# Kernel optimization log

Measured on AMD Instinct MI355X. Metric: run time of the kernel, lower is better.

## Reference

```python
import jax, jax.numpy as jnp
import numpy as np

N = 65536      # occupied voxels
D = 96         # voxel grid extent per axis
CIN = 64
CH = 64
COUT = 16      # 8 * 2
K = 27         # 3^3 kernel offsets


def _build_neighbor_idx(rng):
    # unique occupied voxel coordinates
    lin = rng.choice(D ** 3, size=N, replace=False).astype(np.int64)
    coords = np.stack(np.unravel_index(lin, (D, D, D)), axis=1)  # [N,3]
    grid = np.full(D ** 3, -1, dtype=np.int32)
    grid[lin] = np.arange(N, dtype=np.int32)
    # 27 offsets in {-1,0,1}^3 (MinkowskiEngine kernel map, stride 1)
    offs = np.stack(np.meshgrid(*([np.arange(-1, 2)] * 3), indexing='ij'),
                    axis=-1).reshape(K, 3)
    nc = coords[:, None, :] + offs[None, :, :]            # [N,27,3]
    valid = np.all((nc >= 0) & (nc < D), axis=-1)         # [N,27]
    nlin = (nc[..., 0] * D + nc[..., 1]) * D + nc[..., 2]
    nidx = np.where(valid, grid[np.clip(nlin, 0, D ** 3 - 1)], -1)
    return nidx.astype(np.int32)                          # -1 = no neighbor


def setup_inputs() -> dict:
    key = jax.random.key(0)
    ks = jax.random.split(key, 7)
    rng = np.random.default_rng(0)
    neighbor_idx = jnp.asarray(_build_neighbor_idx(rng))
    s1 = 1.0 / np.sqrt(K * CIN)
    s2 = 1.0 / np.sqrt(K * CH)
    return {
        'x': jax.random.normal(ks[0], (N, CIN), jnp.float32),
        'neighbor_idx': neighbor_idx,
        'W1': jax.random.normal(ks[1], (K, CIN, CH), jnp.float32) * s1,
        'b1': jax.random.normal(ks[2], (CH,), jnp.float32) * 0.1,
        'W2': jax.random.normal(ks[3], (K, CH, CH), jnp.float32) * s2,
        'b2': jax.random.normal(ks[4], (CH,), jnp.float32) * 0.1,
        'W3': jax.random.normal(ks[5], (K, CH, COUT), jnp.float32) * s2,
        'b3': jax.random.normal(ks[6], (COUT,), jnp.float32) * 0.1,
    }


def _sparse_conv(feat, W, b, nidx):
    # feat: [N,Cin], W: [K,Cin,Cout], nidx: [N,K] with -1 for missing
    mask = nidx >= 0
    gathered = jnp.where(mask[..., None],
                         feat[jnp.clip(nidx, 0)], 0.0)    # [N,K,Cin]
    return jnp.einsum('nkc,kcd->nd', gathered, W) + b


def reference(x, neighbor_idx, W1, b1, W2, b2, W3, b3):
    h = jax.nn.relu(_sparse_conv(x, W1, b1, neighbor_idx))
    h = jax.nn.relu(_sparse_conv(h, W2, b2, neighbor_idx))
    return _sparse_conv(h, W3, b3, neighbor_idx)
```

## Files before the change

### kernel.cpp

```cpp
#include <hip/hip_runtime.h>
#include <hip/hip_bf16.h>
#include <stdint.h>

#define N_VOX 65536
#define NK 27
#define BR 64

typedef float f32x4 __attribute__((ext_vector_type(4)));
typedef __bf16 bf16x8 __attribute__((ext_vector_type(8)));

#define WAITVM(n) asm volatile("s_waitcnt vmcnt(" #n ")" ::: "memory")

__device__ __forceinline__ void barrier_fence() {
    asm volatile("" ::: "memory");
    __builtin_amdgcn_s_barrier();
    asm volatile("" ::: "memory");
}

__device__ __forceinline__ void gll16(const void* src, uint32_t lds_addr) {
    asm volatile("s_mov_b32 m0, %0\n\t"
                 "global_load_lds_dwordx4 %1, off"
                 :: "s"(lds_addr), "v"(src)
                 : "memory");
}

__device__ __forceinline__ void wconv_elem(const float* __restrict__ W,
                                           __bf16* __restrict__ Wt, int Dc, int i) {
    int d = i % Dc;
    int c = (i / Dc) % 64;
    int k = i / (Dc * 64);
    int off = ((d * 128 + ((c >> 3) << 4)) ^ ((d & 7) << 4)) + (c & 7) * 2;
    *(__bf16*)((char*)Wt + (size_t)k * Dc * 128 + off) = (__bf16)W[i];
}

#define PREP_CVT   2048
#define PREP_W1    432
#define PREP_W2    432
#define PREP_W3    108
#define PREP_GRID  (PREP_CVT + PREP_W1 + PREP_W2 + PREP_W3 + 1)
__global__ __launch_bounds__(256) void prep_kernel(
    const float* __restrict__ x,
    const float* __restrict__ W1, const float* __restrict__ W2, const float* __restrict__ W3,
    __bf16* __restrict__ xb, __bf16* __restrict__ Wt1, __bf16* __restrict__ Wt2,
    __bf16* __restrict__ Wt3, float* __restrict__ zp)
{
    const int b = blockIdx.x, tid = threadIdx.x;
    if (b < PREP_CVT) {
        int i = b * 256 + tid;
        const f32x4* xp = (const f32x4*)x;
        f32x4 f0 = xp[i * 2], f1 = xp[i * 2 + 1];
        bf16x8 v;
#pragma unroll
        for (int j = 0; j < 4; ++j) { v[j] = (__bf16)f0[j]; v[4 + j] = (__bf16)f1[j]; }
        ((bf16x8*)xb)[i] = v;
    } else if (b < PREP_CVT + PREP_W1) {
        wconv_elem(W1, Wt1, 64, (b - PREP_CVT) * 256 + tid);
    } else if (b < PREP_CVT + PREP_W1 + PREP_W2) {
        wconv_elem(W2, Wt2, 64, (b - PREP_CVT - PREP_W1) * 256 + tid);
    } else if (b < PREP_CVT + PREP_W1 + PREP_W2 + PREP_W3) {
        wconv_elem(W3, Wt3, 16, (b - PREP_CVT - PREP_W1 - PREP_W2) * 256 + tid);
    } else {
        if (tid < 16) ((f32x4*)zp)[tid] = (f32x4){0.f, 0.f, 0.f, 0.f};
    }
}

template <int NCOLS, bool RELU, bool OUT_F32>
__global__ __launch_bounds__(256, 4) void conv_layer(
    const __bf16* __restrict__ feat,
    const int* __restrict__ nidx,
    const __bf16* __restrict__ Wt,
    const float* __restrict__ bias,
    void* __restrict__ dst,
    const __bf16* __restrict__ zp)
{
    constexpr int NI = NCOLS / 16;
    constexpr int BSZ = NCOLS * 128;
    constexpr int BOFF = 2 * BR * 128;
    constexpr int SNOFF = BOFF + 2 * BSZ;
    __shared__ __align__(16) char lds[SNOFF + BR * NK * 4];

    const int tid = threadIdx.x;
    const int lane = tid & 63;
    const int wid = tid >> 6;
    const int col = lane & 15;
    const int kgrp = lane >> 4;
    const int row0 = blockIdx.x * BR;

    int* snid = (int*)(lds + SNOFF);
    const int* gnid = nidx + (size_t)row0 * NK;
    for (int i = tid; i < BR * NK; i += 256) {
        int r = i / NK;
        int kk = i - r * NK;
        snid[kk * BR + r] = gnid[i];
    }
    __syncthreads();

    const uint32_t ldsbase = (uint32_t)(uintptr_t)(&lds[0]);
    const int uw = __builtin_amdgcn_readfirstlane(wid);

    int rA[2], qA[2];
#pragma unroll
    for (int j = 0; j < 2; ++j) {
        int o = (wid * 2 + j) * 1024 + lane * 16;
        rA[j] = o >> 7;
        qA[j] = ((o >> 4) & 7) ^ (rA[j] & 7);
    }

    auto issue = [&](int k, int buf) {
#pragma unroll
        for (int j = 0; j < 2; ++j) {
            int m = snid[k * BR + rA[j]];
            const __bf16* src = (m >= 0) ? (feat + (size_t)m * 64 + qA[j] * 8) : zp;
            uint32_t la = ldsbase + buf * (BR * 128) + (wid * 2 + j) * 1024;
            gll16(src, (uint32_t)__builtin_amdgcn_readfirstlane((int)la));
        }
        if (NCOLS == 64) {
#pragma unroll
            for (int j = 0; j < 2; ++j) {
                int jb = wid * 2 + j;
                const __bf16* src = Wt + (size_t)k * (NCOLS * 64) + jb * 512 + lane * 8;
                uint32_t la = ldsbase + BOFF + buf * BSZ + jb * 1024;
                gll16(src, (uint32_t)__builtin_amdgcn_readfirstlane((int)la));
            }
        } else {
            if (uw < 2) {
                const __bf16* src = Wt + (size_t)k * (NCOLS * 64) + wid * 512 + lane * 8;
                uint32_t la = ldsbase + BOFF + buf * BSZ + wid * 1024;
                gll16(src, (uint32_t)__builtin_amdgcn_readfirstlane((int)la));
            }
        }
    };

    f32x4 acc[NI];
#pragma unroll
    for (int ni = 0; ni < NI; ++ni)
#pragma unroll
        for (int j = 0; j < 4; ++j) acc[ni][j] = 0.f;

    issue(0, 0);

    for (int k = 0; k < NK; ++k) {
        const int cur = k & 1;
        barrier_fence();
        if (k + 1 < NK) {
            issue(k + 1, cur ^ 1);
            if (NCOLS == 64) { WAITVM(4); }
            else { if (uw < 2) { WAITVM(3); } else { WAITVM(2); } }
        } else {
            WAITVM(0);
        }
        barrier_fence();

        const char* Ac = lds + cur * (BR * 128);
        const char* Bc = lds + BOFF + cur * BSZ;
        const int ar = wid * 16 + col;
        bf16x8 a[2];
#pragma unroll
        for (int kk = 0; kk < 2; ++kk)
            a[kk] = *(const bf16x8*)(Ac + ((ar * 128 + kk * 64 + kgrp * 16) ^ ((ar & 7) << 4)));
#pragma unroll
        for (int kk = 0; kk < 2; ++kk)
#pragma unroll
            for (int ni = 0; ni < NI; ++ni) {
                const int br = ni * 16 + col;
                bf16x8 b = *(const bf16x8*)(Bc + ((br * 128 + kk * 64 + kgrp * 16) ^ ((br & 7) << 4)));
                acc[ni] = __builtin_amdgcn_mfma_f32_16x16x32_bf16(a[kk], b, acc[ni], 0, 0, 0);
            }
    }

#pragma unroll
    for (int ni = 0; ni < NI; ++ni) {
        float bv = bias[ni * 16 + col];
#pragma unroll
        for (int reg = 0; reg < 4; ++reg) {
            int r = row0 + wid * 16 + kgrp * 4 + reg;
            float v = acc[ni][reg] + bv;
            if (RELU) v = fmaxf(v, 0.f);
            if (OUT_F32) ((float*)dst)[(size_t)r * NCOLS + ni * 16 + col] = v;
            else ((__bf16*)dst)[(size_t)r * NCOLS + ni * 16 + col] = (__bf16)v;
        }
    }
}

extern "C" void kernel_launch(void* const* d_in, const int* in_sizes, int n_in,
                              void* d_out, int out_size, void* d_ws, size_t ws_size,
                              hipStream_t stream) {
    const float* x  = (const float*)d_in[0];
    const int* nidx = (const int*)d_in[1];
    const float* W1 = (const float*)d_in[2];
    const float* b1 = (const float*)d_in[3];
    const float* W2 = (const float*)d_in[4];
    const float* b2 = (const float*)d_in[5];
    const float* W3 = (const float*)d_in[6];
    const float* b3 = (const float*)d_in[7];

    char* ws = (char*)d_ws;
    __bf16* buf0 = (__bf16*)ws;
    __bf16* buf1 = (__bf16*)(ws + 8388608);
    __bf16* Wt1  = (__bf16*)(ws + 16777216);
    __bf16* Wt2  = Wt1 + 27 * 64 * 64;
    __bf16* Wt3  = Wt2 + 27 * 64 * 64;
    __bf16* zp   = Wt3 + 27 * 16 * 64;

    prep_kernel<<<PREP_GRID, 256, 0, stream>>>(x, W1, W2, W3, buf0, Wt1, Wt2, Wt3, (float*)zp);

    dim3 grid(N_VOX / BR);
    conv_layer<64, true,  false><<<grid, 256, 0, stream>>>(buf0, nidx, Wt1, b1, buf1, zp);
    conv_layer<64, true,  false><<<grid, 256, 0, stream>>>(buf1, nidx, Wt2, b2, buf0, zp);
    conv_layer<16, false, true ><<<grid, 256, 0, stream>>>(buf0, nidx, Wt3, b3, d_out, zp);
}
```

Baseline: 73.40 us.

## Gather A fragments straight into registers and split waves 2x2 for 64-col layers

Neighbor feature rows are now loaded directly from global memory into registers in MFMA fragment layout, instead of going through LDS with global_load_lds. Only the weights stay in double-buffered LDS. The A fragments are double-buffered in registers across an unrolled two-step loop with explicit vmcnt waits, and the 64-column layers use a 2x2 wave tiling so each wave reuses its A fragments over two N tiles. This removes the LDS traffic for A and one LDS round trip per kernel offset, at the cost of more VGPRs and per-lane scattered 16-byte loads.

```diff
diff --git a/kernel.cpp b/kernel.cpp
--- a/kernel.cpp
+++ b/kernel.cpp
@@ -22,6 +22,14 @@
                  "global_load_lds_dwordx4 %1, off"
                  :: "s"(lds_addr), "v"(src)
                  : "memory");
+}
+
+__device__ __forceinline__ f32x4 gload16(const void* src) {
+    f32x4 r;
+    uint64_t ad = (uint64_t)(uintptr_t)src;
+    asm volatile("global_load_dwordx4 %0, %1, off"
+                 : "=v"(r) : "v"(ad) : "memory");
+    return r;
 }
 
 __device__ __forceinline__ void wconv_elem(const float* __restrict__ W,
@@ -73,15 +81,19 @@
     void* __restrict__ dst,
     const __bf16* __restrict__ zp)
 {
-    constexpr int NI = NCOLS / 16;
+    constexpr int WC = (NCOLS == 64) ? 2 : 1;
+    constexpr int WR = 4 / WC;
+    constexpr int MI = BR / (WR * 16);
+    constexpr int NI = NCOLS / (WC * 16);
     constexpr int BSZ = NCOLS * 128;
-    constexpr int BOFF = 2 * BR * 128;
-    constexpr int SNOFF = BOFF + 2 * BSZ;
+    constexpr int SNOFF = 2 * BSZ;
     __shared__ __align__(16) char lds[SNOFF + BR * NK * 4];
 
     const int tid = threadIdx.x;
     const int lane = tid & 63;
     const int wid = tid >> 6;
+    const int wr = wid / WC;
+    const int wc = wid % WC;
     const int col = lane & 15;
     const int kgrp = lane >> 4;
     const int row0 = blockIdx.x * BR;
@@ -97,87 +109,118 @@
 
     const uint32_t ldsbase = (uint32_t)(uintptr_t)(&lds[0]);
     const int uw = __builtin_amdgcn_readfirstlane(wid);
-
-    int rA[2], qA[2];
-#pragma unroll
-    for (int j = 0; j < 2; ++j) {
-        int o = (wid * 2 + j) * 1024 + lane * 16;
-        rA[j] = o >> 7;
-        qA[j] = ((o >> 4) & 7) ^ (rA[j] & 7);
-    }
-
-    auto issue = [&](int k, int buf) {
-#pragma unroll
-        for (int j = 0; j < 2; ++j) {
-            int m = snid[k * BR + rA[j]];
-            const __bf16* src = (m >= 0) ? (feat + (size_t)m * 64 + qA[j] * 8) : zp;
-            uint32_t la = ldsbase + buf * (BR * 128) + (wid * 2 + j) * 1024;
-            gll16(src, (uint32_t)__builtin_amdgcn_readfirstlane((int)la));
-        }
-        if (NCOLS == 64) {
+    const char* featB = (const char*)feat;
+    const char* zpB = (const char*)zp;
+    const int chunk = kgrp * 16;
+
+    auto issueB = [&](int k, int p) {
+        if constexpr (NCOLS == 64) {
 #pragma unroll
             for (int j = 0; j < 2; ++j) {
                 int jb = wid * 2 + j;
                 const __bf16* src = Wt + (size_t)k * (NCOLS * 64) + jb * 512 + lane * 8;
-                uint32_t la = ldsbase + BOFF + buf * BSZ + jb * 1024;
-                gll16(src, (uint32_t)__builtin_amdgcn_readfirstlane((int)la));
+                gll16(src, (uint32_t)__builtin_amdgcn_readfirstlane(
+                                (int)(ldsbase + p * BSZ + jb * 1024)));
             }
         } else {
             if (uw < 2) {
                 const __bf16* src = Wt + (size_t)k * (NCOLS * 64) + wid * 512 + lane * 8;
-                uint32_t la = ldsbase + BOFF + buf * BSZ + wid * 1024;
-                gll16(src, (uint32_t)__builtin_amdgcn_readfirstlane((int)la));
+                gll16(src, (uint32_t)__builtin_amdgcn_readfirstlane(
+                                (int)(ldsbase + p * BSZ + wid * 1024)));
             }
         }
     };
 
-    f32x4 acc[NI];
-#pragma unroll
-    for (int ni = 0; ni < NI; ++ni)
-#pragma unroll
-        for (int j = 0; j < 4; ++j) acc[ni][j] = 0.f;
-
-    issue(0, 0);
-
-    for (int k = 0; k < NK; ++k) {
-        const int cur = k & 1;
+    auto issueA = [&](int k, f32x4 (&a)[MI][2]) {
+#pragma unroll
+        for (int mi = 0; mi < MI; ++mi) {
+            int r = wr * (MI * 16) + mi * 16 + col;
+            int m = snid[k * BR + r];
+            const char* base = (m >= 0) ? (featB + (size_t)m * 128) : zpB;
+#pragma unroll
+            for (int kk = 0; kk < 2; ++kk)
+                a[mi][kk] = gload16(base + kk * 64 + chunk);
+        }
+    };
+
+    f32x4 acc[MI][NI];
+#pragma unroll
+    for (int mi = 0; mi < MI; ++mi)
+#pragma unroll
+        for (int ni = 0; ni < NI; ++ni)
+#pragma unroll
+            for (int j = 0; j < 4; ++j) acc[mi][ni][j] = 0.f;
+
+    auto compute = [&](int k, f32x4 (&a)[MI][2]) {
+        const char* Bc = lds + (k & 1) * BSZ;
+        bf16x8 b[NI][2];
+#pragma unroll
+        for (int ni = 0; ni < NI; ++ni) {
+            int br = wc * (NI * 16) + ni * 16 + col;
+#pragma unroll
+            for (int kk = 0; kk < 2; ++kk)
+                b[ni][kk] = *(const bf16x8*)(Bc + ((br * 128 + kk * 64 + kgrp * 16)
+                                                   ^ ((br & 7) << 4)));
+        }
+#pragma unroll
+        for (int kk = 0; kk < 2; ++kk)
+#pragma unroll
+            for (int mi = 0; mi < MI; ++mi)
+#pragma unroll
+                for (int ni = 0; ni < NI; ++ni)
+                    acc[mi][ni] = __builtin_amdgcn_mfma_f32_16x16x32_bf16(
+                        __builtin_bit_cast(bf16x8, a[mi][kk]), b[ni][kk],
+                        acc[mi][ni], 0, 0, 0);
+    };
+
+#define WAIT_TOP() do { if constexpr (NCOLS == 64) { WAITVM(4); } else { WAITVM(2); } } while (0)
+#define WAIT_MID() do { if constexpr (NCOLS == 64) { WAITVM(6); } \
+                        else { if (uw < 2) { WAITVM(3); } else { WAITVM(2); } } } while (0)
+
+    f32x4 aA[MI][2], aB[MI][2];
+    issueB(0, 0);
+    issueA(0, aA);
+
+    for (int k2 = 0; k2 < 13; ++k2) {
+        const int k = 2 * k2;
+        WAIT_TOP();
         barrier_fence();
-        if (k + 1 < NK) {
-            issue(k + 1, cur ^ 1);
-            if (NCOLS == 64) { WAITVM(4); }
-            else { if (uw < 2) { WAITVM(3); } else { WAITVM(2); } }
-        } else {
-            WAITVM(0);
-        }
+        issueB(k + 1, (k + 1) & 1);
+        issueA(k + 1, aB);
+        WAIT_MID();
+        __builtin_amdgcn_sched_barrier(0);
+        compute(k, aA);
+        WAIT_TOP();
         barrier_fence();
-
-        const char* Ac = lds + cur * (BR * 128);
-        const char* Bc = lds + BOFF + cur * BSZ;
-        const int ar = wid * 16 + col;
-        bf16x8 a[2];
-#pragma unroll
-        for (int kk = 0; kk < 2; ++kk)
-            a[kk] = *(const bf16x8*)(Ac + ((ar * 128 + kk * 64 + kgrp * 16) ^ ((ar & 7) << 4)));
-#pragma unroll
-        for (int kk = 0; kk < 2; ++kk)
-#pragma unroll
-            for (int ni = 0; ni < NI; ++ni) {
-                const int br = ni * 16 + col;
-                bf16x8 b = *(const bf16x8*)(Bc + ((br * 128 + kk * 64 + kgrp * 16) ^ ((br & 7) << 4)));
-                acc[ni] = __builtin_amdgcn_mfma_f32_16x16x32_bf16(a[kk], b, acc[ni], 0, 0, 0);
+        issueB(k + 2, (k + 2) & 1);
+        issueA(k + 2, aA);
+        WAIT_MID();
+        __builtin_amdgcn_sched_barrier(0);
+        compute(k + 1, aB);
+    }
+    WAIT_TOP();
+    barrier_fence();
+    WAITVM(0);
+    __builtin_amdgcn_sched_barrier(0);
+    compute(26, aA);
+
+#undef WAIT_TOP
+#undef WAIT_MID
+
+#pragma unroll
+    for (int ni = 0; ni < NI; ++ni) {
+        float bv = bias[wc * (NI * 16) + ni * 16 + col];
+#pragma unroll
+        for (int mi = 0; mi < MI; ++mi) {
+#pragma unroll
+            for (int reg = 0; reg < 4; ++reg) {
+                int r = row0 + wr * (MI * 16) + mi * 16 + kgrp * 4 + reg;
+                int c = wc * (NI * 16) + ni * 16 + col;
+                float v = acc[mi][ni][reg] + bv;
+                if (RELU) v = fmaxf(v, 0.f);
+                if (OUT_F32) ((float*)dst)[(size_t)r * NCOLS + c] = v;
+                else ((__bf16*)dst)[(size_t)r * NCOLS + c] = (__bf16)v;
             }
-    }
-
-#pragma unroll
-    for (int ni = 0; ni < NI; ++ni) {
-        float bv = bias[ni * 16 + col];
-#pragma unroll
-        for (int reg = 0; reg < 4; ++reg) {
-            int r = row0 + wid * 16 + kgrp * 4 + reg;
-            float v = acc[ni][reg] + bv;
-            if (RELU) v = fmaxf(v, 0.f);
-            if (OUT_F32) ((float*)dst)[(size_t)r * NCOLS + ni * 16 + col] = v;
-            else ((__bf16*)dst)[(size_t)r * NCOLS + ni * 16 + col] = (__bf16)v;
         }
     }
 }
```

New measurement: 88.43 us. 20.5% more time.

## Double conv row tile to 128 with two M sub-tiles per wave

Applied to the files above, without the earlier changes.

Each conv block now handles 128 voxel rows instead of 64, and each wave computes two 16-row MFMA sub-tiles that share every loaded weight fragment. The per-offset weight tile is loaded into LDS once per 128 rows, so weight traffic and barriers per row are halved. Weight loads are now issued before the gathered feature loads, and the vmcnt waits are adjusted for four gather loads per wave. The cost is more LDS and registers per block, so occupancy hint drops to 2 blocks per CU and the grid shrinks to 512 blocks, which may reduce latency hiding for the irregular gathers.

```diff
diff --git a/kernel.cpp b/kernel.cpp
--- a/kernel.cpp
+++ b/kernel.cpp
@@ -4,7 +4,7 @@
 
 #define N_VOX 65536
 #define NK 27
-#define BR 64
+#define BR 128
 
 typedef float f32x4 __attribute__((ext_vector_type(4)));
 typedef __bf16 bf16x8 __attribute__((ext_vector_type(8)));
@@ -65,7 +65,7 @@
 }
 
 template <int NCOLS, bool RELU, bool OUT_F32>
-__global__ __launch_bounds__(256, 4) void conv_layer(
+__global__ __launch_bounds__(256, 2) void conv_layer(
     const __bf16* __restrict__ feat,
     const int* __restrict__ nidx,
     const __bf16* __restrict__ Wt,
@@ -73,9 +73,11 @@
     void* __restrict__ dst,
     const __bf16* __restrict__ zp)
 {
+    constexpr int MI = 2;
     constexpr int NI = NCOLS / 16;
+    constexpr int ABSZ = BR * 128;
     constexpr int BSZ = NCOLS * 128;
-    constexpr int BOFF = 2 * BR * 128;
+    constexpr int BOFF = 2 * ABSZ;
     constexpr int SNOFF = BOFF + 2 * BSZ;
     __shared__ __align__(16) char lds[SNOFF + BR * NK * 4];
 
@@ -98,44 +100,46 @@
     const uint32_t ldsbase = (uint32_t)(uintptr_t)(&lds[0]);
     const int uw = __builtin_amdgcn_readfirstlane(wid);
 
-    int rA[2], qA[2];
-#pragma unroll
-    for (int j = 0; j < 2; ++j) {
-        int o = (wid * 2 + j) * 1024 + lane * 16;
+    int rA[4], qA[4];
+#pragma unroll
+    for (int j = 0; j < 4; ++j) {
+        int o = (wid * 4 + j) * 1024 + lane * 16;
         rA[j] = o >> 7;
         qA[j] = ((o >> 4) & 7) ^ (rA[j] & 7);
     }
 
     auto issue = [&](int k, int buf) {
-#pragma unroll
-        for (int j = 0; j < 2; ++j) {
-            int m = snid[k * BR + rA[j]];
-            const __bf16* src = (m >= 0) ? (feat + (size_t)m * 64 + qA[j] * 8) : zp;
-            uint32_t la = ldsbase + buf * (BR * 128) + (wid * 2 + j) * 1024;
-            gll16(src, (uint32_t)__builtin_amdgcn_readfirstlane((int)la));
-        }
-        if (NCOLS == 64) {
+        if constexpr (NCOLS == 64) {
 #pragma unroll
             for (int j = 0; j < 2; ++j) {
                 int jb = wid * 2 + j;
                 const __bf16* src = Wt + (size_t)k * (NCOLS * 64) + jb * 512 + lane * 8;
-                uint32_t la = ldsbase + BOFF + buf * BSZ + jb * 1024;
-                gll16(src, (uint32_t)__builtin_amdgcn_readfirstlane((int)la));
+                gll16(src, (uint32_t)__builtin_amdgcn_readfirstlane(
+                                (int)(ldsbase + BOFF + buf * BSZ + jb * 1024)));
             }
         } else {
             if (uw < 2) {
                 const __bf16* src = Wt + (size_t)k * (NCOLS * 64) + wid * 512 + lane * 8;
-                uint32_t la = ldsbase + BOFF + buf * BSZ + wid * 1024;
-                gll16(src, (uint32_t)__builtin_amdgcn_readfirstlane((int)la));
-            }
+                gll16(src, (uint32_t)__builtin_amdgcn_readfirstlane(
+                                (int)(ldsbase + BOFF + buf * BSZ + wid * 1024)));
+            }
+        }
+#pragma unroll
+        for (int j = 0; j < 4; ++j) {
+            int m = snid[k * BR + rA[j]];
+            const __bf16* src = (m >= 0) ? (feat + (size_t)m * 64 + qA[j] * 8) : zp;
+            gll16(src, (uint32_t)__builtin_amdgcn_readfirstlane(
+                            (int)(ldsbase + buf * ABSZ + (wid * 4 + j) * 1024)));
         }
     };
 
-    f32x4 acc[NI];
-#pragma unroll
-    for (int ni = 0; ni < NI; ++ni)
-#pragma unroll
-        for (int j = 0; j < 4; ++j) acc[ni][j] = 0.f;
+    f32x4 acc[MI][NI];
+#pragma unroll
+    for (int mi = 0; mi < MI; ++mi)
+#pragma unroll
+        for (int ni = 0; ni < NI; ++ni)
+#pragma unroll
+            for (int j = 0; j < 4; ++j) acc[mi][ni][j] = 0.f;
 
     issue(0, 0);
 
@@ -144,27 +148,35 @@
         barrier_fence();
         if (k + 1 < NK) {
             issue(k + 1, cur ^ 1);
-            if (NCOLS == 64) { WAITVM(4); }
-            else { if (uw < 2) { WAITVM(3); } else { WAITVM(2); } }
+            if constexpr (NCOLS == 64) { WAITVM(6); }
+            else { if (uw < 2) { WAITVM(5); } else { WAITVM(4); } }
         } else {
             WAITVM(0);
         }
         barrier_fence();
 
-        const char* Ac = lds + cur * (BR * 128);
+        const char* Ac = lds + cur * ABSZ;
         const char* Bc = lds + BOFF + cur * BSZ;
-        const int ar = wid * 16 + col;
-        bf16x8 a[2];
+        bf16x8 a[MI][2];
+#pragma unroll
+        for (int mi = 0; mi < MI; ++mi) {
+            int ar = wid * 32 + mi * 16 + col;
+#pragma unroll
+            for (int kk = 0; kk < 2; ++kk)
+                a[mi][kk] = *(const bf16x8*)(Ac + ((ar * 128 + kk * 64 + kgrp * 16)
+                                                   ^ ((ar & 7) << 4)));
+        }
 #pragma unroll
         for (int kk = 0; kk < 2; ++kk)
-            a[kk] = *(const bf16x8*)(Ac + ((ar * 128 + kk * 64 + kgrp * 16) ^ ((ar & 7) << 4)));
-#pragma unroll
-        for (int kk = 0; kk < 2; ++kk)
 #pragma unroll
             for (int ni = 0; ni < NI; ++ni) {
-                const int br = ni * 16 + col;
-                bf16x8 b = *(const bf16x8*)(Bc + ((br * 128 + kk * 64 + kgrp * 16) ^ ((br & 7) << 4)));
-                acc[ni] = __builtin_amdgcn_mfma_f32_16x16x32_bf16(a[kk], b, acc[ni], 0, 0, 0);
+                int br = ni * 16 + col;
+                bf16x8 b = *(const bf16x8*)(Bc + ((br * 128 + kk * 64 + kgrp * 16)
+                                                  ^ ((br & 7) << 4)));
+#pragma unroll
+                for (int mi = 0; mi < MI; ++mi)
+                    acc[mi][ni] = __builtin_amdgcn_mfma_f32_16x16x32_bf16(
+                        a[mi][kk], b, acc[mi][ni], 0, 0, 0);
             }
     }
 
@@ -172,12 +184,15 @@
     for (int ni = 0; ni < NI; ++ni) {
         float bv = bias[ni * 16 + col];
 #pragma unroll
-        for (int reg = 0; reg < 4; ++reg) {
-            int r = row0 + wid * 16 + kgrp * 4 + reg;
-            float v = acc[ni][reg] + bv;
-            if (RELU) v = fmaxf(v, 0.f);
-            if (OUT_F32) ((float*)dst)[(size_t)r * NCOLS + ni * 16 + col] = v;
-            else ((__bf16*)dst)[(size_t)r * NCOLS + ni * 16 + col] = (__bf16)v;
+        for (int mi = 0; mi < MI; ++mi) {
+#pragma unroll
+            for (int reg = 0; reg < 4; ++reg) {
+                int r = row0 + wid * 32 + mi * 16 + kgrp * 4 + reg;
+                float v = acc[mi][ni][reg] + bv;
+                if (RELU) v = fmaxf(v, 0.f);
+                if (OUT_F32) ((float*)dst)[(size_t)r * NCOLS + ni * 16 + col] = v;
+                else ((__bf16*)dst)[(size_t)r * NCOLS + ni * 16 + col] = (__bf16)v;
+            }
         }
     }
 }
```

After: 75.59 us. 1.03x slower.
